# Optimization experiments

Measured on AMD Instinct MI355X. Metric: run time of the kernel, lower is better.

## Reference

```python
import jax, jax.numpy as jnp
import numpy as np

EMB = 192
HEADS = 6
WIN = (8, 8)
N = WIN[0] * WIN[1]  # 64
B_ = 2048
NW = 1024  # mask windows per image; B_ % NW == 0


def _relative_position_index():
    coords_h = np.arange(WIN[0])
    coords_w = np.arange(WIN[1])
    coords = np.stack(np.meshgrid(coords_h, coords_w, indexing='ij'))  # (2,Wh,Ww)
    cf = coords.reshape(2, -1)
    rel = cf[:, :, None] - cf[:, None, :]  # (2,N,N)
    rel = rel.transpose(1, 2, 0)
    rel[:, :, 0] += WIN[0] - 1
    rel[:, :, 1] += WIN[1] - 1
    rel[:, :, 0] *= 2 * WIN[1] - 1
    return rel.sum(-1).astype(np.int32)  # (N,N)


def setup_inputs() -> dict:
    key = jax.random.key(0)
    ks = jax.random.split(key, 12)
    num_bias = (2 * WIN[0] - 1) * (2 * WIN[1] - 1)  # 225
    s = 0.02
    return {
        'q': jax.random.normal(ks[0], (B_, N, EMB), jnp.float32),
        'k': jax.random.normal(ks[1], (B_, N, EMB), jnp.float32),
        'v': jax.random.normal(ks[2], (B_, N, EMB), jnp.float32),
        'mask': jax.random.normal(ks[3], (NW, N, N), jnp.float32),
        'Wq': jax.random.normal(ks[4], (EMB, EMB), jnp.float32) * s,
        'bq': jnp.zeros((EMB,), jnp.float32),
        'Wk': jax.random.normal(ks[5], (EMB, EMB), jnp.float32) * s,
        'bk': jnp.zeros((EMB,), jnp.float32),
        'Wv': jax.random.normal(ks[6], (EMB, EMB), jnp.float32) * s,
        'bv': jnp.zeros((EMB,), jnp.float32),
        'Wp': jax.random.normal(ks[7], (EMB, EMB), jnp.float32) * s,
        'bp': jnp.zeros((EMB,), jnp.float32),
        'bias_table': jax.random.normal(ks[8], (num_bias, HEADS), jnp.float32) * s,
        'rel_index': jnp.asarray(_relative_position_index()),
    }


def reference(q, k, v, mask, Wq, bq, Wk, bk, Wv, bv, Wp, bp, bias_table, rel_index):
    head_dim = EMB // HEADS
    scale = head_dim ** -0.5

    def split_heads(x):
        # (B_,N,C) -> (B_,H,N,D)
        return x.reshape(B_, N, HEADS, head_dim).transpose(0, 2, 1, 3)

    qh = split_heads(q @ Wq + bq) * scale
    kh = split_heads(k @ Wk + bk)
    vh = split_heads(v @ Wv + bv)

    attn = jnp.einsum('bhnd,bhmd->bhnm', qh, kh)  # (B_,H,N,N)

    # gathered relative position bias: (N,N,H) -> (H,N,N)
    rel_bias = bias_table[rel_index.reshape(-1)].reshape(N, N, HEADS).transpose(2, 0, 1)
    attn = attn + rel_bias[None]

    # mask add: reshape to (B, nW, H, N, N) and broadcast mask over batch/heads
    nW = mask.shape[0]
    attn = attn.reshape(-1, nW, HEADS, N, N) + mask[None, :, None]
    attn = attn.reshape(-1, HEADS, N, N)
    attn = jax.nn.softmax(attn, axis=-1)

    x = jnp.einsum('bhnm,bhmd->bhnd', attn, vh)  # (B_,H,N,D)
    x = x.transpose(0, 2, 1, 3).reshape(B_, N, EMB)
    x = x @ Wp + bp
    return (x, attn)
```

## Files before the change

kernel.cpp:

```cpp
#include <hip/hip_runtime.h>
#include <hip/hip_bf16.h>

typedef __attribute__((ext_vector_type(8))) short   bf16x8;
typedef __attribute__((ext_vector_type(4))) float   f32x4;
typedef __attribute__((ext_vector_type(4))) unsigned short u16x4;
typedef unsigned short u16;

#define NTOK 64
#define CEMB 192
#define NH   6
#define PADC 200
#define VPAD 72

__device__ __forceinline__ u16 f2b(float f) {
  unsigned u = __float_as_uint(f);
  unsigned r = (u + 0x7fffu + ((u >> 16) & 1u)) >> 16;
  return (u16)r;
}

__global__ void prep_kernel(const float* __restrict__ Wq, const float* __restrict__ Wk,
                            const float* __restrict__ Wv, const float* __restrict__ Wp,
                            const float* __restrict__ btab, const int* __restrict__ ridx,
                            u16* __restrict__ WT, float* __restrict__ rb) {
  int idx = blockIdx.x * 256 + threadIdx.x;
  if (idx < 4 * 36864) {
    int m = idx / 36864;
    int e = idx - m * 36864;
    int n = e / CEMB;
    int k = e - n * CEMB;
    const float* W = (m == 0) ? Wq : (m == 1) ? Wk : (m == 2) ? Wv : Wp;
    WT[idx] = f2b(W[k * CEMB + n]);
  } else {
    int i2 = idx - 4 * 36864;
    if (i2 < NH * 4096) {
      int h = i2 >> 12;
      int ij = i2 & 4095;
      rb[i2] = btab[ridx[ij] * NH + h];
    }
  }
}

__global__ __launch_bounds__(512, 2)
void wattn_kernel(const float* __restrict__ qg, const float* __restrict__ kg,
                  const float* __restrict__ vg, const float* __restrict__ maskg,
                  const float* __restrict__ bq, const float* __restrict__ bk,
                  const float* __restrict__ bv, const float* __restrict__ bp,
                  const u16* __restrict__ WT, const float* __restrict__ rb,
                  float* __restrict__ xout, float* __restrict__ attn_out) {
  __shared__ u16 sQ[NTOK * PADC];
  __shared__ u16 sK[NTOK * PADC];
  __shared__ u16 sV[CEMB * VPAD];
  __shared__ u16 sX[NTOK * PADC];
  __shared__ u16 sP[8 * 16 * VPAD];

  const int tid  = threadIdx.x;
  const int wave = tid >> 6;
  const int lane = tid & 63;
  const int l15  = lane & 15;
  const int lhi  = lane >> 4;
  const int b    = blockIdx.x;
  const float scale = 0.17677669529663687f;

  {
    const size_t base = (size_t)b * NTOK * CEMB;
    #pragma unroll
    for (int m = 0; m < 3; ++m) {
      const float* src = (m == 0 ? qg : m == 1 ? kg : vg) + base;
      u16* dst = (m == 0 ? sQ : m == 1 ? sK : sV);
      #pragma unroll
      for (int it = 0; it < 6; ++it) {
        int fi  = it * 512 + tid;
        int row = fi / 48;
        int c4  = (fi - row * 48) * 4;
        const float4 v4 = reinterpret_cast<const float4*>(src)[fi];
        u16x4 p;
        p.x = f2b(v4.x); p.y = f2b(v4.y); p.z = f2b(v4.z); p.w = f2b(v4.w);
        *reinterpret_cast<u16x4*>(&dst[row * PADC + c4]) = p;
      }
    }
  }
  __syncthreads();

  f32x4 accv[5][4];
  #pragma unroll
  for (int si = 0; si < 5; ++si) {
    int strip = wave + si * 8;
    if (strip < 36) {
      int m  = strip / 12;
      int ct = strip - m * 12;
      const u16* Xs = (m == 0) ? sQ : (m == 1) ? sK : sV;
      const u16* Wt = WT + m * 36864 + (ct * 16 + l15) * CEMB + lhi * 8;
      f32x4 z = {0.f, 0.f, 0.f, 0.f};
      #pragma unroll
      for (int rt = 0; rt < 4; ++rt) accv[si][rt] = z;
      #pragma unroll
      for (int ks = 0; ks < 6; ++ks) {
        bf16x8 bw = *reinterpret_cast<const bf16x8*>(Wt + ks * 32);
        #pragma unroll
        for (int rt = 0; rt < 4; ++rt) {
          bf16x8 ax = *reinterpret_cast<const bf16x8*>(&Xs[(rt * 16 + l15) * PADC + ks * 32 + lhi * 8]);
          accv[si][rt] = __builtin_amdgcn_mfma_f32_16x16x32_bf16(ax, bw, accv[si][rt], 0, 0, 0);
        }
      }
    }
  }
  __syncthreads();

  #pragma unroll
  for (int si = 0; si < 5; ++si) {
    int strip = wave + si * 8;
    if (strip < 36) {
      int m  = strip / 12;
      int ct = strip - m * 12;
      int n  = ct * 16 + l15;
      float bval = ((m == 0) ? bq : (m == 1) ? bk : bv)[n];
      if (m == 0) {
        #pragma unroll
        for (int rt = 0; rt < 4; ++rt)
          #pragma unroll
          for (int r = 0; r < 4; ++r)
            sQ[(rt * 16 + lhi * 4 + r) * PADC + n] = f2b((accv[si][rt][r] + bval) * scale);
      } else if (m == 1) {
        #pragma unroll
        for (int rt = 0; rt < 4; ++rt)
          #pragma unroll
          for (int r = 0; r < 4; ++r)
            sK[(rt * 16 + lhi * 4 + r) * PADC + n] = f2b(accv[si][rt][r] + bval);
      } else {
        #pragma unroll
        for (int rt = 0; rt < 4; ++rt)
          #pragma unroll
          for (int r = 0; r < 4; ++r)
            sV[n * VPAD + rt * 16 + lhi * 4 + r] = f2b(accv[si][rt][r] + bval);
      }
    }
  }
  __syncthreads();

  const float* maskw = maskg + (size_t)(b & 1023) * 4096;
  u16* pw = sP + wave * 16 * VPAD;
  #pragma unroll
  for (int ui = 0; ui < 3; ++ui) {
    int u  = wave + ui * 8;
    int h  = u >> 2;
    int rt = u & 3;
    int irow = rt * 16 + lhi * 4;

    bf16x8 aq = *reinterpret_cast<const bf16x8*>(&sQ[(rt * 16 + l15) * PADC + h * 32 + lhi * 8]);
    f32x4 sv[4];
    #pragma unroll
    for (int ct = 0; ct < 4; ++ct) {
      bf16x8 bkf = *reinterpret_cast<const bf16x8*>(&sK[(ct * 16 + l15) * PADC + h * 32 + lhi * 8]);
      f32x4 z = {0.f, 0.f, 0.f, 0.f};
      sv[ct] = __builtin_amdgcn_mfma_f32_16x16x32_bf16(aq, bkf, z, 0, 0, 0);
    }

    const float* rbp = rb + h * 4096 + irow * 64 + l15;
    const float* mkp = maskw + irow * 64 + l15;
    float lg[4][4];
    #pragma unroll
    for (int ct = 0; ct < 4; ++ct)
      #pragma unroll
      for (int r = 0; r < 4; ++r)
        lg[ct][r] = sv[ct][r] + rbp[r * 64 + ct * 16] + mkp[r * 64 + ct * 16];

    float pr[4][4];
    #pragma unroll
    for (int r = 0; r < 4; ++r) {
      float mx = fmaxf(fmaxf(lg[0][r], lg[1][r]), fmaxf(lg[2][r], lg[3][r]));
      mx = fmaxf(mx, __shfl_xor(mx, 1));
      mx = fmaxf(mx, __shfl_xor(mx, 2));
      mx = fmaxf(mx, __shfl_xor(mx, 4));
      mx = fmaxf(mx, __shfl_xor(mx, 8));
      float e0 = __expf(lg[0][r] - mx), e1 = __expf(lg[1][r] - mx);
      float e2 = __expf(lg[2][r] - mx), e3 = __expf(lg[3][r] - mx);
      float sum = e0 + e1 + e2 + e3;
      sum += __shfl_xor(sum, 1);
      sum += __shfl_xor(sum, 2);
      sum += __shfl_xor(sum, 4);
      sum += __shfl_xor(sum, 8);
      float inv = 1.0f / sum;
      pr[0][r] = e0 * inv; pr[1][r] = e1 * inv; pr[2][r] = e2 * inv; pr[3][r] = e3 * inv;
    }

    float* ap = attn_out + (((size_t)b * NH + h) * NTOK + irow) * NTOK;
    #pragma unroll
    for (int ct = 0; ct < 4; ++ct)
      #pragma unroll
      for (int r = 0; r < 4; ++r) {
        ap[r * 64 + ct * 16 + l15] = pr[ct][r];
        pw[(lhi * 4 + r) * VPAD + ct * 16 + l15] = f2b(pr[ct][r]);
      }

    f32x4 xa[2];
    {
      f32x4 z = {0.f, 0.f, 0.f, 0.f};
      xa[0] = z; xa[1] = z;
    }
    #pragma unroll
    for (int ks = 0; ks < 2; ++ks) {
      bf16x8 apf = *reinterpret_cast<const bf16x8*>(&pw[l15 * VPAD + ks * 32 + lhi * 8]);
      #pragma unroll
      for (int ctv = 0; ctv < 2; ++ctv) {
        bf16x8 bvf = *reinterpret_cast<const bf16x8*>(&sV[(h * 32 + ctv * 16 + l15) * VPAD + ks * 32 + lhi * 8]);
        xa[ctv] = __builtin_amdgcn_mfma_f32_16x16x32_bf16(apf, bvf, xa[ctv], 0, 0, 0);
      }
    }
    #pragma unroll
    for (int ctv = 0; ctv < 2; ++ctv)
      #pragma unroll
      for (int r = 0; r < 4; ++r)
        sX[(rt * 16 + lhi * 4 + r) * PADC + h * 32 + ctv * 16 + l15] = f2b(xa[ctv][r]);
  }
  __syncthreads();

  #pragma unroll
  for (int ui = 0; ui < 3; ++ui) {
    int u2 = wave + ui * 8;
    int ct = u2 % 12;
    int rh = u2 / 12;
    const u16* Wt = WT + 3 * 36864 + (ct * 16 + l15) * CEMB + lhi * 8;
    f32x4 oa[2];
    {
      f32x4 z = {0.f, 0.f, 0.f, 0.f};
      oa[0] = z; oa[1] = z;
    }
    #pragma unroll
    for (int ks = 0; ks < 6; ++ks) {
      bf16x8 bw = *reinterpret_cast<const bf16x8*>(Wt + ks * 32);
      #pragma unroll
      for (int rr = 0; rr < 2; ++rr) {
        bf16x8 ax = *reinterpret_cast<const bf16x8*>(&sX[(rh * 32 + rr * 16 + l15) * PADC + ks * 32 + lhi * 8]);
        oa[rr] = __builtin_amdgcn_mfma_f32_16x16x32_bf16(ax, bw, oa[rr], 0, 0, 0);
      }
    }
    float bias = bp[ct * 16 + l15];
    #pragma unroll
    for (int rr = 0; rr < 2; ++rr)
      #pragma unroll
      for (int r = 0; r < 4; ++r)
        xout[((size_t)b * NTOK + rh * 32 + rr * 16 + lhi * 4 + r) * CEMB + ct * 16 + l15] = oa[rr][r] + bias;
  }
}

extern "C" void kernel_launch(void* const* d_in, const int* in_sizes, int n_in,
                              void* d_out, int out_size, void* d_ws, size_t ws_size,
                              hipStream_t stream) {
  const float* q    = (const float*)d_in[0];
  const float* k    = (const float*)d_in[1];
  const float* v    = (const float*)d_in[2];
  const float* mask = (const float*)d_in[3];
  const float* Wq   = (const float*)d_in[4];
  const float* bq   = (const float*)d_in[5];
  const float* Wk   = (const float*)d_in[6];
  const float* bk   = (const float*)d_in[7];
  const float* Wv   = (const float*)d_in[8];
  const float* bv   = (const float*)d_in[9];
  const float* Wp   = (const float*)d_in[10];
  const float* bp   = (const float*)d_in[11];
  const float* btab = (const float*)d_in[12];
  const int*   ridx = (const int*)d_in[13];

  u16*   WT = (u16*)d_ws;
  float* rb = (float*)((char*)d_ws + 4 * 36864 * 2);

  float* xout = (float*)d_out;
  float* attn = xout + (size_t)2048 * NTOK * CEMB;

  prep_kernel<<<672, 256, 0, stream>>>(Wq, Wk, Wv, Wp, btab, ridx, WT, rb);
  wattn_kernel<<<2048, 512, 0, stream>>>(q, k, v, mask, bq, bk, bv, bp, WT, rb, xout, attn);
}
```

Baseline: 242.1 us.

## Swizzle LDS layout, reuse sQ for output, shrink shared memory for higher occupancy

Measured after the change: 221.4 us. -8.5%, faster.

```diff
diff --git a/kernel.cpp b/kernel.cpp
--- a/kernel.cpp
+++ b/kernel.cpp
@@ -9,13 +9,17 @@
 #define NTOK 64
 #define CEMB 192
 #define NH   6
-#define PADC 200
-#define VPAD 72
+#define ROWB 384
+#define VROWB 128
 
 __device__ __forceinline__ u16 f2b(float f) {
   unsigned u = __float_as_uint(f);
   unsigned r = (u + 0x7fffu + ((u >> 16) & 1u)) >> 16;
   return (u16)r;
+}
+
+__device__ __forceinline__ int swz(int row, int colbyte) {
+  return colbyte ^ ((((row >> 3) ^ row) & 7) << 4);
 }
 
 __global__ void prep_kernel(const float* __restrict__ Wq, const float* __restrict__ Wk,
@@ -40,24 +44,23 @@
   }
 }
 
-__global__ __launch_bounds__(512, 2)
+__global__ __launch_bounds__(512, 4)
 void wattn_kernel(const float* __restrict__ qg, const float* __restrict__ kg,
                   const float* __restrict__ vg, const float* __restrict__ maskg,
                   const float* __restrict__ bq, const float* __restrict__ bk,
                   const float* __restrict__ bv, const float* __restrict__ bp,
                   const u16* __restrict__ WT, const float* __restrict__ rb,
                   float* __restrict__ xout, float* __restrict__ attn_out) {
-  __shared__ u16 sQ[NTOK * PADC];
-  __shared__ u16 sK[NTOK * PADC];
-  __shared__ u16 sV[CEMB * VPAD];
-  __shared__ u16 sX[NTOK * PADC];
-  __shared__ u16 sP[8 * 16 * VPAD];
-
+  __shared__ __align__(16) char smem[81920];
+  char* sQ = smem;
+  char* sK = smem + 24576;
+  char* sV = smem + 49152;
   const int tid  = threadIdx.x;
   const int wave = tid >> 6;
   const int lane = tid & 63;
   const int l15  = lane & 15;
   const int lhi  = lane >> 4;
+  char* sP = smem + 73728 + wave * 1024;
   const int b    = blockIdx.x;
   const float scale = 0.17677669529663687f;
 
@@ -66,16 +69,16 @@
     #pragma unroll
     for (int m = 0; m < 3; ++m) {
       const float* src = (m == 0 ? qg : m == 1 ? kg : vg) + base;
-      u16* dst = (m == 0 ? sQ : m == 1 ? sK : sV);
+      char* dst = (m == 0 ? sQ : m == 1 ? sK : sV);
       #pragma unroll
       for (int it = 0; it < 6; ++it) {
         int fi  = it * 512 + tid;
         int row = fi / 48;
-        int c4  = (fi - row * 48) * 4;
+        int ce  = (fi - row * 48) * 4;
         const float4 v4 = reinterpret_cast<const float4*>(src)[fi];
         u16x4 p;
         p.x = f2b(v4.x); p.y = f2b(v4.y); p.z = f2b(v4.z); p.w = f2b(v4.w);
-        *reinterpret_cast<u16x4*>(&dst[row * PADC + c4]) = p;
+        *reinterpret_cast<u16x4*>(dst + row * ROWB + swz(row, ce * 2)) = p;
       }
     }
   }
@@ -88,7 +91,7 @@
     if (strip < 36) {
       int m  = strip / 12;
       int ct = strip - m * 12;
-      const u16* Xs = (m == 0) ? sQ : (m == 1) ? sK : sV;
+      const char* Xs = (m == 0) ? sQ : (m == 1) ? sK : sV;
       const u16* Wt = WT + m * 36864 + (ct * 16 + l15) * CEMB + lhi * 8;
       f32x4 z = {0.f, 0.f, 0.f, 0.f};
       #pragma unroll
@@ -98,7 +101,8 @@
         bf16x8 bw = *reinterpret_cast<const bf16x8*>(Wt + ks * 32);
         #pragma unroll
         for (int rt = 0; rt < 4; ++rt) {
-          bf16x8 ax = *reinterpret_cast<const bf16x8*>(&Xs[(rt * 16 + l15) * PADC + ks * 32 + lhi * 8]);
+          int row = rt * 16 + l15;
+          bf16x8 ax = *reinterpret_cast<const bf16x8*>(Xs + row * ROWB + swz(row, ks * 64 + lhi * 16));
           accv[si][rt] = __builtin_amdgcn_mfma_f32_16x16x32_bf16(ax, bw, accv[si][rt], 0, 0, 0);
         }
       }
@@ -118,27 +122,33 @@
         #pragma unroll
         for (int rt = 0; rt < 4; ++rt)
           #pragma unroll
-          for (int r = 0; r < 4; ++r)
-            sQ[(rt * 16 + lhi * 4 + r) * PADC + n] = f2b((accv[si][rt][r] + bval) * scale);
+          for (int r = 0; r < 4; ++r) {
+            int row = rt * 16 + lhi * 4 + r;
+            *reinterpret_cast<u16*>(sQ + row * ROWB + swz(row, n * 2)) = f2b((accv[si][rt][r] + bval) * scale);
+          }
       } else if (m == 1) {
         #pragma unroll
         for (int rt = 0; rt < 4; ++rt)
           #pragma unroll
-          for (int r = 0; r < 4; ++r)
-            sK[(rt * 16 + lhi * 4 + r) * PADC + n] = f2b(accv[si][rt][r] + bval);
+          for (int r = 0; r < 4; ++r) {
+            int row = rt * 16 + lhi * 4 + r;
+            *reinterpret_cast<u16*>(sK + row * ROWB + swz(row, n * 2)) = f2b(accv[si][rt][r] + bval);
+          }
       } else {
         #pragma unroll
-        for (int rt = 0; rt < 4; ++rt)
+        for (int rt = 0; rt < 4; ++rt) {
+          int t0 = rt * 16 + lhi * 4;
+          u16x4 pk;
           #pragma unroll
-          for (int r = 0; r < 4; ++r)
-            sV[n * VPAD + rt * 16 + lhi * 4 + r] = f2b(accv[si][rt][r] + bval);
+          for (int r = 0; r < 4; ++r) pk[r] = f2b(accv[si][rt][r] + bval);
+          *reinterpret_cast<u16x4*>(sV + n * VROWB + swz(n, t0 * 2)) = pk;
+        }
       }
     }
   }
   __syncthreads();
 
   const float* maskw = maskg + (size_t)(b & 1023) * 4096;
-  u16* pw = sP + wave * 16 * VPAD;
   #pragma unroll
   for (int ui = 0; ui < 3; ++ui) {
     int u  = wave + ui * 8;
@@ -146,23 +156,34 @@
     int rt = u & 3;
     int irow = rt * 16 + lhi * 4;
 
-    bf16x8 aq = *reinterpret_cast<const bf16x8*>(&sQ[(rt * 16 + l15) * PADC + h * 32 + lhi * 8]);
+    const float* rbp = rb + h * 4096 + irow * 64 + l15;
+    const float* mkp = maskw + irow * 64 + l15;
+    float rbv[4][4], mkv[4][4];
+    #pragma unroll
+    for (int ct = 0; ct < 4; ++ct)
+      #pragma unroll
+      for (int r = 0; r < 4; ++r) {
+        rbv[ct][r] = rbp[r * 64 + ct * 16];
+        mkv[ct][r] = mkp[r * 64 + ct * 16];
+      }
+
+    int qrow = rt * 16 + l15;
+    bf16x8 aq = *reinterpret_cast<const bf16x8*>(sQ + qrow * ROWB + swz(qrow, h * 64 + lhi * 16));
     f32x4 sv[4];
     #pragma unroll
     for (int ct = 0; ct < 4; ++ct) {
-      bf16x8 bkf = *reinterpret_cast<const bf16x8*>(&sK[(ct * 16 + l15) * PADC + h * 32 + lhi * 8]);
+      int krow = ct * 16 + l15;
+      bf16x8 bkf = *reinterpret_cast<const bf16x8*>(sK + krow * ROWB + swz(krow, h * 64 + lhi * 16));
       f32x4 z = {0.f, 0.f, 0.f, 0.f};
       sv[ct] = __builtin_amdgcn_mfma_f32_16x16x32_bf16(aq, bkf, z, 0, 0, 0);
     }
 
-    const float* rbp = rb + h * 4096 + irow * 64 + l15;
-    const float* mkp = maskw + irow * 64 + l15;
     float lg[4][4];
     #pragma unroll
     for (int ct = 0; ct < 4; ++ct)
       #pragma unroll
       for (int r = 0; r < 4; ++r)
-        lg[ct][r] = sv[ct][r] + rbp[r * 64 + ct * 16] + mkp[r * 64 + ct * 16];
+        lg[ct][r] = sv[ct][r] + rbv[ct][r] + mkv[ct][r];
 
     float pr[4][4];
     #pragma unroll
@@ -187,30 +208,40 @@
     #pragma unroll
     for (int ct = 0; ct < 4; ++ct)
       #pragma unroll
+      for (int r = 0; r < 4; ++r)
+        ap[r * 64 + ct * 16 + l15] = pr[ct][r];
+
+    f32x4 xa[2];
+    { f32x4 z = {0.f, 0.f, 0.f, 0.f}; xa[0] = z; xa[1] = z; }
+    #pragma unroll
+    for (int ks = 0; ks < 2; ++ks) {
+      #pragma unroll
+      for (int c = 0; c < 2; ++c)
+        #pragma unroll
+        for (int r = 0; r < 4; ++r) {
+          int col  = c * 16 + l15;
+          int kg   = col >> 3;
+          int j    = col & 7;
+          int prow = lhi * 4 + r;
+          *reinterpret_cast<u16*>(sP + ((kg * 16 + prow) * 8 + j) * 2) = f2b(pr[ks * 2 + c][r]);
+        }
+      bf16x8 apf = *reinterpret_cast<const bf16x8*>(sP + lane * 16);
+      #pragma unroll
+      for (int ctv = 0; ctv < 2; ++ctv) {
+        int vrow = h * 32 + ctv * 16 + l15;
+        bf16x8 bvf = *reinterpret_cast<const bf16x8*>(sV + vrow * VROWB + swz(vrow, ks * 64 + lhi * 16));
+        xa[ctv] = __builtin_amdgcn_mfma_f32_16x16x32_bf16(apf, bvf, xa[ctv], 0, 0, 0);
+      }
+    }
+
+    #pragma unroll
+    for (int ctv = 0; ctv < 2; ++ctv)
+      #pragma unroll
       for (int r = 0; r < 4; ++r) {
-        ap[r * 64 + ct * 16 + l15] = pr[ct][r];
-        pw[(lhi * 4 + r) * VPAD + ct * 16 + l15] = f2b(pr[ct][r]);
-      }
-
-    f32x4 xa[2];
-    {
-      f32x4 z = {0.f, 0.f, 0.f, 0.f};
-      xa[0] = z; xa[1] = z;
-    }
-    #pragma unroll
-    for (int ks = 0; ks < 2; ++ks) {
-      bf16x8 apf = *reinterpret_cast<const bf16x8*>(&pw[l15 * VPAD + ks * 32 + lhi * 8]);
-      #pragma unroll
-      for (int ctv = 0; ctv < 2; ++ctv) {
-        bf16x8 bvf = *reinterpret_cast<const bf16x8*>(&sV[(h * 32 + ctv * 16 + l15) * VPAD + ks * 32 + lhi * 8]);
-        xa[ctv] = __builtin_amdgcn_mfma_f32_16x16x32_bf16(apf, bvf, xa[ctv], 0, 0, 0);
-      }
-    }
-    #pragma unroll
-    for (int ctv = 0; ctv < 2; ++ctv)
-      #pragma unroll
-      for (int r = 0; r < 4; ++r)
-        sX[(rt * 16 + lhi * 4 + r) * PADC + h * 32 + ctv * 16 + l15] = f2b(xa[ctv][r]);
+        int xrow = rt * 16 + lhi * 4 + r;
+        int xcol = h * 32 + ctv * 16 + l15;
+        *reinterpret_cast<u16*>(sQ + xrow * ROWB + swz(xrow, xcol * 2)) = f2b(xa[ctv][r]);
+      }
   }
   __syncthreads();
 
@@ -221,16 +252,14 @@
     int rh = u2 / 12;
     const u16* Wt = WT + 3 * 36864 + (ct * 16 + l15) * CEMB + lhi * 8;
     f32x4 oa[2];
-    {
-      f32x4 z = {0.f, 0.f, 0.f, 0.f};
-      oa[0] = z; oa[1] = z;
-    }
+    { f32x4 z = {0.f, 0.f, 0.f, 0.f}; oa[0] = z; oa[1] = z; }
     #pragma unroll
     for (int ks = 0; ks < 6; ++ks) {
       bf16x8 bw = *reinterpret_cast<const bf16x8*>(Wt + ks * 32);
       #pragma unroll
       for (int rr = 0; rr < 2; ++rr) {
-        bf16x8 ax = *reinterpret_cast<const bf16x8*>(&sX[(rh * 32 + rr * 16 + l15) * PADC + ks * 32 + lhi * 8]);
+        int xrow = rh * 32 + rr * 16 + l15;
+        bf16x8 ax = *reinterpret_cast<const bf16x8*>(sQ + xrow * ROWB + swz(xrow, ks * 64 + lhi * 16));
         oa[rr] = __builtin_amdgcn_mfma_f32_16x16x32_bf16(ax, bw, oa[rr], 0, 0, 0);
       }
     }
```

## Cut LDS footprint: load QKV straight into MFMA fragments, keep Q in registers, swizzle LDS

Applied to the files above, without the earlier changes.

After: 444.0 us. 83.4% more time.

```diff
diff --git a/kernel.cpp b/kernel.cpp
--- a/kernel.cpp
+++ b/kernel.cpp
@@ -3,19 +3,30 @@
 
 typedef __attribute__((ext_vector_type(8))) short   bf16x8;
 typedef __attribute__((ext_vector_type(4))) float   f32x4;
-typedef __attribute__((ext_vector_type(4))) unsigned short u16x4;
 typedef unsigned short u16;
 
 #define NTOK 64
 #define CEMB 192
 #define NH   6
-#define PADC 200
-#define VPAD 72
+#define ROWB 384
+#define VROWB 128
+
+union U8 { uint4 u; bf16x8 v; };
 
 __device__ __forceinline__ u16 f2b(float f) {
   unsigned u = __float_as_uint(f);
   unsigned r = (u + 0x7fffu + ((u >> 16) & 1u)) >> 16;
   return (u16)r;
+}
+
+__device__ __forceinline__ unsigned cvtpk(float lo, float hi) {
+  unsigned r;
+  asm("v_cvt_pk_bf16_f32 %0, %1, %2" : "=v"(r) : "v"(lo), "v"(hi));
+  return r;
+}
+
+__device__ __forceinline__ int swz(int row, int colbyte) {
+  return colbyte ^ ((((row >> 3) ^ row) & 7) << 4);
 }
 
 __global__ void prep_kernel(const float* __restrict__ Wq, const float* __restrict__ Wk,
@@ -40,117 +51,121 @@
   }
 }
 
-__global__ __launch_bounds__(512, 2)
+__global__ __launch_bounds__(512, 6)
 void wattn_kernel(const float* __restrict__ qg, const float* __restrict__ kg,
                   const float* __restrict__ vg, const float* __restrict__ maskg,
                   const float* __restrict__ bq, const float* __restrict__ bk,
                   const float* __restrict__ bv, const float* __restrict__ bp,
                   const u16* __restrict__ WT, const float* __restrict__ rb,
                   float* __restrict__ xout, float* __restrict__ attn_out) {
-  __shared__ u16 sQ[NTOK * PADC];
-  __shared__ u16 sK[NTOK * PADC];
-  __shared__ u16 sV[CEMB * VPAD];
-  __shared__ u16 sX[NTOK * PADC];
-  __shared__ u16 sP[8 * 16 * VPAD];
-
+  __shared__ __align__(16) char smem[53248];
+  char* sK  = smem;
+  char* sVT = smem + 24576;
   const int tid  = threadIdx.x;
   const int wave = tid >> 6;
   const int lane = tid & 63;
   const int l15  = lane & 15;
   const int lhi  = lane >> 4;
-  const int b    = blockIdx.x;
-  const float scale = 0.17677669529663687f;
-
+  char* sS = smem + 49152 + wave * 512;
+  const int b   = blockIdx.x;
+  const int rt  = wave & 3;
+  const int par = wave >> 2;
+  const int irow = rt * 16 + lhi * 4;
+
+  const size_t gbase = (size_t)b * 12288 + (size_t)(rt * 16 + l15) * CEMB + lhi * 8;
+
+  f32x4 qc[6];
   {
-    const size_t base = (size_t)b * NTOK * CEMB;
-    #pragma unroll
-    for (int m = 0; m < 3; ++m) {
-      const float* src = (m == 0 ? qg : m == 1 ? kg : vg) + base;
-      u16* dst = (m == 0 ? sQ : m == 1 ? sK : sV);
-      #pragma unroll
-      for (int it = 0; it < 6; ++it) {
-        int fi  = it * 512 + tid;
-        int row = fi / 48;
-        int c4  = (fi - row * 48) * 4;
-        const float4 v4 = reinterpret_cast<const float4*>(src)[fi];
-        u16x4 p;
-        p.x = f2b(v4.x); p.y = f2b(v4.y); p.z = f2b(v4.z); p.w = f2b(v4.w);
-        *reinterpret_cast<u16x4*>(&dst[row * PADC + c4]) = p;
+    bf16x8 qa[6];
+    #pragma unroll
+    for (int ks = 0; ks < 6; ++ks) {
+      float4 a0 = *reinterpret_cast<const float4*>(qg + gbase + ks * 32);
+      float4 a1 = *reinterpret_cast<const float4*>(qg + gbase + ks * 32 + 4);
+      U8 u;
+      u.u.x = cvtpk(a0.x, a0.y); u.u.y = cvtpk(a0.z, a0.w);
+      u.u.z = cvtpk(a1.x, a1.y); u.u.w = cvtpk(a1.z, a1.w);
+      qa[ks] = u.v;
+    }
+    #pragma unroll
+    for (int s = 0; s < 6; ++s) {
+      int strip = 4 * (s >> 1) + 2 * par + (s & 1);
+      const u16* Wt = WT + (strip * 16 + l15) * CEMB + lhi * 8;
+      f32x4 acc = {0.f, 0.f, 0.f, 0.f};
+      #pragma unroll
+      for (int ks = 0; ks < 6; ++ks)
+        acc = __builtin_amdgcn_mfma_f32_16x16x32_bf16(qa[ks], *reinterpret_cast<const bf16x8*>(Wt + ks * 32), acc, 0, 0, 0);
+      float bb = bq[strip * 16 + l15];
+      #pragma unroll
+      for (int r = 0; r < 4; ++r) qc[s][r] = (acc[r] + bb) * 0.17677669529663687f;
+    }
+  }
+  #pragma unroll
+  for (int m = 1; m < 3; ++m) {
+    const float* src = (m == 1) ? kg : vg;
+    const float* bias = (m == 1) ? bk : bv;
+    bf16x8 xa6[6];
+    #pragma unroll
+    for (int ks = 0; ks < 6; ++ks) {
+      float4 a0 = *reinterpret_cast<const float4*>(src + gbase + ks * 32);
+      float4 a1 = *reinterpret_cast<const float4*>(src + gbase + ks * 32 + 4);
+      U8 u;
+      u.u.x = cvtpk(a0.x, a0.y); u.u.y = cvtpk(a0.z, a0.w);
+      u.u.z = cvtpk(a1.x, a1.y); u.u.w = cvtpk(a1.z, a1.w);
+      xa6[ks] = u.v;
+    }
+    #pragma unroll
+    for (int s = 0; s < 6; ++s) {
+      int strip = par * 6 + s;
+      const u16* Wt = WT + m * 36864 + (strip * 16 + l15) * CEMB + lhi * 8;
+      f32x4 acc = {0.f, 0.f, 0.f, 0.f};
+      #pragma unroll
+      for (int ks = 0; ks < 6; ++ks)
+        acc = __builtin_amdgcn_mfma_f32_16x16x32_bf16(xa6[ks], *reinterpret_cast<const bf16x8*>(Wt + ks * 32), acc, 0, 0, 0);
+      float bb = bias[strip * 16 + l15];
+      if (m == 1) {
+        #pragma unroll
+        for (int r = 0; r < 4; ++r) {
+          int row = rt * 16 + lhi * 4 + r;
+          *reinterpret_cast<u16*>(sK + row * ROWB + swz(row, (strip * 16 + l15) * 2)) = f2b(acc[r] + bb);
+        }
+      } else {
+        int chan = strip * 16 + l15;
+        #pragma unroll
+        for (int r = 0; r < 4; ++r) {
+          int tok = rt * 16 + lhi * 4 + r;
+          *reinterpret_cast<u16*>(sVT + chan * VROWB + swz(chan, tok * 2)) = f2b(acc[r] + bb);
+        }
       }
     }
   }
   __syncthreads();
 
-  f32x4 accv[5][4];
+  const float* maskw = maskg + (size_t)(b & 1023) * 4096;
+
   #pragma unroll
-  for (int si = 0; si < 5; ++si) {
-    int strip = wave + si * 8;
-    if (strip < 36) {
-      int m  = strip / 12;
-      int ct = strip - m * 12;
-      const u16* Xs = (m == 0) ? sQ : (m == 1) ? sK : sV;
-      const u16* Wt = WT + m * 36864 + (ct * 16 + l15) * CEMB + lhi * 8;
-      f32x4 z = {0.f, 0.f, 0.f, 0.f};
-      #pragma unroll
-      for (int rt = 0; rt < 4; ++rt) accv[si][rt] = z;
-      #pragma unroll
-      for (int ks = 0; ks < 6; ++ks) {
-        bf16x8 bw = *reinterpret_cast<const bf16x8*>(Wt + ks * 32);
-        #pragma unroll
-        for (int rt = 0; rt < 4; ++rt) {
-          bf16x8 ax = *reinterpret_cast<const bf16x8*>(&Xs[(rt * 16 + l15) * PADC + ks * 32 + lhi * 8]);
-          accv[si][rt] = __builtin_amdgcn_mfma_f32_16x16x32_bf16(ax, bw, accv[si][rt], 0, 0, 0);
-        }
-      }
-    }
-  }
-  __syncthreads();
-
-  #pragma unroll
-  for (int si = 0; si < 5; ++si) {
-    int strip = wave + si * 8;
-    if (strip < 36) {
-      int m  = strip / 12;
-      int ct = strip - m * 12;
-      int n  = ct * 16 + l15;
-      float bval = ((m == 0) ? bq : (m == 1) ? bk : bv)[n];
-      if (m == 0) {
-        #pragma unroll
-        for (int rt = 0; rt < 4; ++rt)
-          #pragma unroll
-          for (int r = 0; r < 4; ++r)
-            sQ[(rt * 16 + lhi * 4 + r) * PADC + n] = f2b((accv[si][rt][r] + bval) * scale);
-      } else if (m == 1) {
-        #pragma unroll
-        for (int rt = 0; rt < 4; ++rt)
-          #pragma unroll
-          for (int r = 0; r < 4; ++r)
-            sK[(rt * 16 + lhi * 4 + r) * PADC + n] = f2b(accv[si][rt][r] + bval);
-      } else {
-        #pragma unroll
-        for (int rt = 0; rt < 4; ++rt)
-          #pragma unroll
-          for (int r = 0; r < 4; ++r)
-            sV[n * VPAD + rt * 16 + lhi * 4 + r] = f2b(accv[si][rt][r] + bval);
-      }
-    }
-  }
-  __syncthreads();
-
-  const float* maskw = maskg + (size_t)(b & 1023) * 4096;
-  u16* pw = sP + wave * 16 * VPAD;
-  #pragma unroll
-  for (int ui = 0; ui < 3; ++ui) {
-    int u  = wave + ui * 8;
-    int h  = u >> 2;
-    int rt = u & 3;
-    int irow = rt * 16 + lhi * 4;
-
-    bf16x8 aq = *reinterpret_cast<const bf16x8*>(&sQ[(rt * 16 + l15) * PADC + h * 32 + lhi * 8]);
+  for (int ri = 0; ri < 3; ++ri) {
+    int h = 2 * ri + par;
+
+    #pragma unroll
+    for (int r = 0; r < 4; ++r)
+      *reinterpret_cast<u16*>(sS + ((lhi * 4 + r) * 16 + l15) * 2) = f2b(qc[2 * ri][r]);
+    U8 h0; h0.u = *reinterpret_cast<const uint4*>(sS + l15 * 32 + (lhi & 1) * 16);
+    #pragma unroll
+    for (int r = 0; r < 4; ++r)
+      *reinterpret_cast<u16*>(sS + ((lhi * 4 + r) * 16 + l15) * 2) = f2b(qc[2 * ri + 1][r]);
+    U8 h1; h1.u = *reinterpret_cast<const uint4*>(sS + l15 * 32 + (lhi & 1) * 16);
+    U8 av;
+    av.u.x = (lhi >= 2) ? h1.u.x : h0.u.x;
+    av.u.y = (lhi >= 2) ? h1.u.y : h0.u.y;
+    av.u.z = (lhi >= 2) ? h1.u.z : h0.u.z;
+    av.u.w = (lhi >= 2) ? h1.u.w : h0.u.w;
+    bf16x8 aq = av.v;
+
     f32x4 sv[4];
     #pragma unroll
     for (int ct = 0; ct < 4; ++ct) {
-      bf16x8 bkf = *reinterpret_cast<const bf16x8*>(&sK[(ct * 16 + l15) * PADC + h * 32 + lhi * 8]);
+      int krow = ct * 16 + l15;
+      bf16x8 bkf = *reinterpret_cast<const bf16x8*>(sK + krow * ROWB + swz(krow, h * 64 + lhi * 16));
       f32x4 z = {0.f, 0.f, 0.f, 0.f};
       sv[ct] = __builtin_amdgcn_mfma_f32_16x16x32_bf16(aq, bkf, z, 0, 0, 0);
     }
@@ -187,30 +202,44 @@
     #pragma unroll
     for (int ct = 0; ct < 4; ++ct)
       #pragma unroll
+      for (int r = 0; r < 4; ++r)
+        ap[r * 64 + ct * 16 + l15] = pr[ct][r];
+
+    f32x4 xa[2];
+    { f32x4 z = {0.f, 0.f, 0.f, 0.f}; xa[0] = z; xa[1] = z; }
+    #pragma unroll
+    for (int ks = 0; ks < 2; ++ks) {
+      #pragma unroll
+      for (int r = 0; r < 4; ++r)
+        *reinterpret_cast<u16*>(sS + ((lhi * 4 + r) * 16 + l15) * 2) = f2b(pr[2 * ks][r]);
+      U8 p0; p0.u = *reinterpret_cast<const uint4*>(sS + l15 * 32 + (lhi & 1) * 16);
+      #pragma unroll
+      for (int r = 0; r < 4; ++r)
+        *reinterpret_cast<u16*>(sS + ((lhi * 4 + r) * 16 + l15) * 2) = f2b(pr[2 * ks + 1][r]);
+      U8 p1; p1.u = *reinterpret_cast<const uint4*>(sS + l15 * 32 + (lhi & 1) * 16);
+      U8 pv;
+      pv.u.x = (lhi >= 2) ? p1.u.x : p0.u.x;
+      pv.u.y = (lhi >= 2) ? p1.u.y : p0.u.y;
+      pv.u.z = (lhi >= 2) ? p1.u.z : p0.u.z;
+      pv.u.w = (lhi >= 2) ? p1.u.w : p0.u.w;
+      bf16x8 pa = pv.v;
+      #pragma unroll
+      for (int cb = 0; cb < 2; ++cb) {
+        int chan = h * 32 + cb * 16 + l15;
+        bf16x8 bvf = *reinterpret_cast<const bf16x8*>(sVT + chan * VROWB + swz(chan, (ks * 32 + lhi * 8) * 2));
+        xa[cb] = __builtin_amdgcn_mfma_f32_16x16x32_bf16(pa, bvf, xa[cb], 0, 0, 0);
+      }
+    }
+    __syncthreads();
+
+    #pragma unroll
+    for (int cb = 0; cb < 2; ++cb)
+      #pragma unroll
       for (int r = 0; r < 4; ++r) {
-        ap[r * 64 + ct * 16 + l15] = pr[ct][r];
-        pw[(lhi * 4 + r) * VPAD + ct * 16 + l15] = f2b(pr[ct][r]);
-      }
-
-    f32x4 xa[2];
-    {
-      f32x4 z = {0.f, 0.f, 0.f, 0.f};
-      xa[0] = z; xa[1] = z;
-    }
-    #pragma unroll
-    for (int ks = 0; ks < 2; ++ks) {
-      bf16x8 apf = *reinterpret_cast<const bf16x8*>(&pw[l15 * VPAD + ks * 32 + lhi * 8]);
-      #pragma unroll
-      for (int ctv = 0; ctv < 2; ++ctv) {
-        bf16x8 bvf = *reinterpret_cast<const bf16x8*>(&sV[(h * 32 + ctv * 16 + l15) * VPAD + ks * 32 + lhi * 8]);
-        xa[ctv] = __builtin_amdgcn_mfma_f32_16x16x32_bf16(apf, bvf, xa[ctv], 0, 0, 0);
-      }
-    }
-    #pragma unroll
-    for (int ctv = 0; ctv < 2; ++ctv)
-      #pragma unroll
-      for (int r = 0; r < 4; ++r)
-        sX[(rt * 16 + lhi * 4 + r) * PADC + h * 32 + ctv * 16 + l15] = f2b(xa[ctv][r]);
+        int xrow = rt * 16 + lhi * 4 + r;
+        int xcol = h * 32 + cb * 16 + l15;
+        *reinterpret_cast<u16*>(sK + xrow * ROWB + swz(xrow, xcol * 2)) = f2b(xa[cb][r]);
+      }
   }
   __syncthreads();
 
@@ -221,16 +250,14 @@
     int rh = u2 / 12;
     const u16* Wt = WT + 3 * 36864 + (ct * 16 + l15) * CEMB + lhi * 8;
     f32x4 oa[2];
-    {
-      f32x4 z = {0.f, 0.f, 0.f, 0.f};
-      oa[0] = z; oa[1] = z;
-    }
+    { f32x4 z = {0.f, 0.f, 0.f, 0.f}; oa[0] = z; oa[1] = z; }
     #pragma unroll
     for (int ks = 0; ks < 6; ++ks) {
       bf16x8 bw = *reinterpret_cast<const bf16x8*>(Wt + ks * 32);
       #pragma unroll
       for (int rr = 0; rr < 2; ++rr) {
-        bf16x8 ax = *reinterpret_cast<const bf16x8*>(&sX[(rh * 32 + rr * 16 + l15) * PADC + ks * 32 + lhi * 8]);
+        int xrow = rh * 32 + rr * 16 + l15;
+        bf16x8 ax = *reinterpret_cast<const bf16x8*>(sK + xrow * ROWB + swz(xrow, ks * 64 + lhi * 16));
         oa[rr] = __builtin_amdgcn_mfma_f32_16x16x32_bf16(ax, bw, oa[rr], 0, 0, 0);
       }
     }
```
